# Optimization experiments

Measured on AMD Instinct MI355X. Metric: run time of the kernel, lower is better.

## Reference

```python
import jax, jax.numpy as jnp
import numpy as np

IN_C, OUT_C, N = 512, 256, 8192
NEG_INF = -1000000000.0  # matches torch's -1e9 fill


def setup_inputs() -> dict:
    key = jax.random.key(0)
    ks = jax.random.split(key, 8)
    x = jax.random.normal(ks[0], (N, IN_C), dtype=jnp.float32)
    adj = jax.random.randint(ks[1], (N, N), 0, 2, dtype=jnp.int32)
    # fc: Linear(in_c, out_c)
    lim_fc = 1.0 / np.sqrt(IN_C)
    W_fc = jax.random.uniform(ks[2], (IN_C, OUT_C), minval=-lim_fc, maxval=lim_fc, dtype=jnp.float32)
    b_fc = jax.random.uniform(ks[3], (OUT_C,), minval=-lim_fc, maxval=lim_fc, dtype=jnp.float32)
    # a1, a2: Linear(out_c, 1)
    lim_a = 1.0 / np.sqrt(OUT_C)
    W_a1 = jax.random.uniform(ks[4], (OUT_C, 1), minval=-lim_a, maxval=lim_a, dtype=jnp.float32)
    b_a1 = jax.random.uniform(ks[5], (1,), minval=-lim_a, maxval=lim_a, dtype=jnp.float32)
    W_a2 = jax.random.uniform(ks[6], (OUT_C, 1), minval=-lim_a, maxval=lim_a, dtype=jnp.float32)
    b_a2 = jax.random.uniform(ks[7], (1,), minval=-lim_a, maxval=lim_a, dtype=jnp.float32)
    return {"x": x, "adj": adj, "W_fc": W_fc, "b_fc": b_fc,
            "W_a1": W_a1, "b_a1": b_a1, "W_a2": W_a2, "b_a2": b_a2}


def reference(x, adj, W_fc, b_fc, W_a1, b_a1, W_a2, b_a2):
    h = x @ W_fc + b_fc                      # [N, out_c]
    s1 = h @ W_a1 + b_a1                     # [N, 1]
    s2 = h @ W_a2 + b_a2                     # [N, 1]
    e = jax.nn.leaky_relu(s1 + s2.T)         # [N, N], slope 0.01 matches torch default
    att = jnp.where(adj > 0, e, NEG_INF)
    att = jax.nn.softmax(att, axis=1)        # dropout omitted (eval mode)
    return att @ h                           # [N, out_c]
```

## Files before the change

kernel.cpp:

```cpp
#include <hip/hip_runtime.h>
#include <hip/hip_bf16.h>

#define IN_C 512
#define OUT_C 256
#define NN 8192
#define JSPL 4
#define JRANGE (NN / JSPL)
#define NT (JRANGE / 64)

typedef __attribute__((ext_vector_type(8))) short s16x8;
typedef __attribute__((ext_vector_type(4))) float f32x4;

__device__ __forceinline__ ushort f2bf(float f) {
    unsigned u = __float_as_uint(f);
    unsigned r = (u + 0x7FFF + ((u >> 16) & 1)) >> 16;
    return (ushort)r;
}

__device__ __forceinline__ void gload_lds16(const uint4* g, uint4* l) {
    __builtin_amdgcn_global_load_lds(
        (const __attribute__((address_space(1))) unsigned int*)g,
        (__attribute__((address_space(3))) unsigned int*)l, 16, 0, 0);
}

__global__ __launch_bounds__(256) void fc_kernel(
    const float* __restrict__ x, const float* __restrict__ Wfc,
    const float* __restrict__ bfc, const float* __restrict__ Wa1,
    const float* __restrict__ ba1, const float* __restrict__ Wa2,
    const float* __restrict__ ba2,
    uint4* __restrict__ hb,
    float* __restrict__ s1, float* __restrict__ s2)
{
    __shared__ float xl[8 * IN_C];
    __shared__ float red[2][8][4];
    const int t = threadIdx.x;
    const int r0 = blockIdx.x * 8;

    {
        const float4* src = (const float4*)(x + (size_t)r0 * IN_C);
        float4* dst = (float4*)xl;
        #pragma unroll
        for (int i = 0; i < 4; i++) dst[i * 256 + t] = src[i * 256 + t];
    }
    __syncthreads();

    float acc[8];
    #pragma unroll
    for (int r = 0; r < 8; r++) acc[r] = 0.f;

    for (int c4 = 0; c4 < IN_C / 4; c4++) {
        const float w0 = Wfc[(c4 * 4 + 0) * OUT_C + t];
        const float w1 = Wfc[(c4 * 4 + 1) * OUT_C + t];
        const float w2 = Wfc[(c4 * 4 + 2) * OUT_C + t];
        const float w3 = Wfc[(c4 * 4 + 3) * OUT_C + t];
        #pragma unroll
        for (int r = 0; r < 8; r++) {
            const float4 xv = *(const float4*)&xl[r * IN_C + c4 * 4];
            acc[r] = fmaf(xv.x, w0, acc[r]);
            acc[r] = fmaf(xv.y, w1, acc[r]);
            acc[r] = fmaf(xv.z, w2, acc[r]);
            acc[r] = fmaf(xv.w, w3, acc[r]);
        }
    }
    const float bb = bfc[t];
    #pragma unroll
    for (int r = 0; r < 8; r++) acc[r] += bb;

    {
        union { ushort u[8]; uint4 v; } pk;
        #pragma unroll
        for (int r = 0; r < 8; r++) pk.u[r] = f2bf(acc[r]);
        const int jt = r0 >> 6, u = (r0 >> 3) & 7;
        hb[(size_t)jt * 2048 + t * 8 + (u ^ (t & 7))] = pk.v;
    }

    float p1[8], p2[8];
    const float wa1 = Wa1[t], wa2 = Wa2[t];
    #pragma unroll
    for (int r = 0; r < 8; r++) { p1[r] = acc[r] * wa1; p2[r] = acc[r] * wa2; }
    #pragma unroll
    for (int off = 32; off > 0; off >>= 1) {
        #pragma unroll
        for (int r = 0; r < 8; r++) {
            p1[r] += __shfl_down(p1[r], off);
            p2[r] += __shfl_down(p2[r], off);
        }
    }
    const int wv = t >> 6, ln = t & 63;
    if (ln == 0) {
        #pragma unroll
        for (int r = 0; r < 8; r++) { red[0][r][wv] = p1[r]; red[1][r][wv] = p2[r]; }
    }
    __syncthreads();
    if (t < 16) {
        const int s = t >> 3, r = t & 7;
        float v = red[s][r][0] + red[s][r][1] + red[s][r][2] + red[s][r][3];
        v += s ? ba2[0] : ba1[0];
        if (s) s2[r0 + r] = v; else s1[r0 + r] = v;
    }
}

__global__ __launch_bounds__(256) void smax_kernel(const float* __restrict__ s2,
                                                   float* __restrict__ smax)
{
    __shared__ float red[4];
    float m = -1e30f;
    for (int i = threadIdx.x; i < NN; i += 256) m = fmaxf(m, s2[i]);
    #pragma unroll
    for (int off = 32; off > 0; off >>= 1) m = fmaxf(m, __shfl_down(m, off));
    if ((threadIdx.x & 63) == 0) red[threadIdx.x >> 6] = m;
    __syncthreads();
    if (threadIdx.x == 0)
        smax[0] = fmaxf(fmaxf(red[0], red[1]), fmaxf(red[2], red[3]));
}

__global__ __launch_bounds__(256, 2) void attn_kernel(
    const int* __restrict__ adj, const uint4* __restrict__ hb,
    const float* __restrict__ s1, const float* __restrict__ s2,
    const float* __restrict__ smaxp, float* __restrict__ outp,
    float* __restrict__ pbase, float* __restrict__ rs)
{
    __shared__ float s2l[JRANGE];
    __shared__ uint4 hbuf[2][2048];

    const int t = threadIdx.x;
    const int wave = t >> 6, lane = t & 63;
    const int g = lane >> 4, lr = lane & 15;
    const int jq = blockIdx.y;
    const int Jbase = jq * JRANGE;
    const int row = blockIdx.x * 64 + wave * 16 + lr;

    {
        const float4* src = (const float4*)(s2 + Jbase);
        float4* dst = (float4*)s2l;
        #pragma unroll
        for (int i = 0; i < JRANGE / 4 / 256; i++) dst[i * 256 + t] = src[i * 256 + t];
    }

    const float my_s1 = s1[row];
    const float z0 = my_s1 + smaxp[0];
    const float m_i = fmaxf(z0, 0.01f * z0);

    f32x4 acc[16];
    #pragma unroll
    for (int n = 0; n < 16; n++) acc[n] = (f32x4)(0.f);
    float rsum = 0.f;

    const int* adj_row = adj + (size_t)row * NN + Jbase + g * 8;
    const uint4* hb_base = hb + (size_t)(Jbase >> 6) * 2048;
    const int stidx = wave * 512 + lane;

    #pragma unroll
    for (int u = 0; u < 8; u++)
        gload_lds16(hb_base + stidx + u * 64, &hbuf[0][stidx + u * 64]);
    int4 ap0 = *(const int4*)(adj_row);
    int4 ap1 = *(const int4*)(adj_row + 4);
    int4 ap2 = *(const int4*)(adj_row + 32);
    int4 ap3 = *(const int4*)(adj_row + 36);
    __syncthreads();

    for (int tt = 0; tt < NT; ++tt) {
        const int cur = tt & 1;
        const bool more = (tt + 1 < NT);
        if (more) {
            const uint4* gs = hb_base + (size_t)(tt + 1) * 2048 + stidx;
            #pragma unroll
            for (int u = 0; u < 8; u++)
                gload_lds16(gs + u * 64, &hbuf[cur ^ 1][stidx + u * 64]);
        }
        const int av[16] = {ap0.x, ap0.y, ap0.z, ap0.w, ap1.x, ap1.y, ap1.z, ap1.w,
                            ap2.x, ap2.y, ap2.z, ap2.w, ap3.x, ap3.y, ap3.z, ap3.w};
        if (more) {
            const int* anx = adj_row + (tt + 1) * 64;
            ap0 = *(const int4*)(anx);
            ap1 = *(const int4*)(anx + 4);
            ap2 = *(const int4*)(anx + 32);
            ap3 = *(const int4*)(anx + 36);
        }

        const int J = tt * 64;
        #pragma unroll
        for (int s = 0; s < 2; s++) {
            const int j0 = J + s * 32 + g * 8;
            const float4 sva = *(const float4*)(s2l + j0);
            const float4 svb = *(const float4*)(s2l + j0 + 4);
            const float sv[8] = {sva.x, sva.y, sva.z, sva.w, svb.x, svb.y, svb.z, svb.w};
            union { ushort u[8]; s16x8 v; } pk;
            #pragma unroll
            for (int e = 0; e < 8; e++) {
                const float zz = my_s1 + sv[e];
                const float ee = fmaxf(zz, 0.01f * zz);
                float p = __expf(ee - m_i);
                p = (av[s * 8 + e] > 0) ? p : 0.f;
                rsum += p;
                pk.u[e] = f2bf(p);
            }
            const s16x8 afrag = pk.v;
            const int slot = (s * 4 + g) ^ (lr & 7);
            #pragma unroll
            for (int n = 0; n < 16; n++) {
                const int col = n * 16 + lr;
                const s16x8 bfrag = *(const s16x8*)&hbuf[cur][col * 8 + slot];
                acc[n] = __builtin_amdgcn_mfma_f32_16x16x32_bf16(afrag, bfrag, acc[n], 0, 0, 0);
            }
        }
        __syncthreads();
    }

    rsum += __shfl_xor(rsum, 16);
    rsum += __shfl_xor(rsum, 32);
    if (g == 0) rs[(size_t)jq * NN + row] = rsum;

    float* dst = (jq == 0) ? outp : (pbase + (size_t)(jq - 1) * ((size_t)NN * OUT_C));
    #pragma unroll
    for (int r = 0; r < 4; r++) {
        const int orow = blockIdx.x * 64 + wave * 16 + g * 4 + r;
        float* op = dst + (size_t)orow * OUT_C + lr;
        #pragma unroll
        for (int n = 0; n < 16; n++) op[n * 16] = acc[n][r];
    }
}

__global__ __launch_bounds__(256) void combine_kernel(
    float* __restrict__ out, const float* __restrict__ pbase,
    const float* __restrict__ rs)
{
    const int row = blockIdx.x, t = threadIdx.x;
    const float rsum = rs[row] + rs[NN + row] + rs[2 * NN + row] + rs[3 * NN + row];
    const float inv = 1.f / rsum;
    const size_t idx = (size_t)row * OUT_C + t;
    const size_t stride = (size_t)NN * OUT_C;
    const float v = out[idx] + pbase[idx] + pbase[idx + stride] + pbase[idx + 2 * stride];
    out[idx] = v * inv;
}

extern "C" void kernel_launch(void* const* d_in, const int* in_sizes, int n_in,
                              void* d_out, int out_size, void* d_ws, size_t ws_size,
                              hipStream_t stream) {
    const float* x   = (const float*)d_in[0];
    const int*   adj = (const int*)d_in[1];
    const float* Wfc = (const float*)d_in[2];
    const float* bfc = (const float*)d_in[3];
    const float* Wa1 = (const float*)d_in[4];
    const float* ba1 = (const float*)d_in[5];
    const float* Wa2 = (const float*)d_in[6];
    const float* ba2 = (const float*)d_in[7];
    float* out = (float*)d_out;

    char* ws = (char*)d_ws;
    uint4* hb   = (uint4*)ws;
    float* s1   = (float*)(ws + (4u << 20));
    float* s2   = s1 + NN;
    float* rs   = s2 + NN;
    float* smax = rs + 4 * NN;
    float* pbase = (float*)(ws + (5u << 20));

    fc_kernel<<<dim3(NN / 8), 256, 0, stream>>>(x, Wfc, bfc, Wa1, ba1, Wa2, ba2, hb, s1, s2);
    smax_kernel<<<dim3(1), 256, 0, stream>>>(s2, smax);
    attn_kernel<<<dim3(NN / 64, JSPL), 256, 0, stream>>>(adj, hb, s1, s2, smax, out, pbase, rs);
    combine_kernel<<<dim3(NN), 256, 0, stream>>>(out, pbase, rs);
}
```

Before: 180.0 us.

## Pack adjacency matrix into a bitmask before the attention kernel

Measured after the change: 186.2 us. +3.5%, slower.

```diff
diff --git a/kernel.cpp b/kernel.cpp
--- a/kernel.cpp
+++ b/kernel.cpp
@@ -7,6 +7,7 @@
 #define JSPL 4
 #define JRANGE (NN / JSPL)
 #define NT (JRANGE / 64)
+#define CHUNKS_TOTAL (NN * (NN / 256))
 
 typedef __attribute__((ext_vector_type(8))) short s16x8;
 typedef __attribute__((ext_vector_type(4))) float f32x4;
@@ -21,6 +22,26 @@
     __builtin_amdgcn_global_load_lds(
         (const __attribute__((address_space(1))) unsigned int*)g,
         (__attribute__((address_space(3))) unsigned int*)l, 16, 0, 0);
+}
+
+__global__ __launch_bounds__(256) void pack_kernel(const int* __restrict__ adj,
+                                                   unsigned char* __restrict__ mask)
+{
+    const int wid = blockIdx.x * 4 + (threadIdx.x >> 6);
+    const int lane = threadIdx.x & 63;
+    const size_t base = (size_t)wid * 64;
+    #pragma unroll 4
+    for (int i = 0; i < 64; i++) {
+        const size_t ci = base + i;
+        const int4 a = ((const int4*)adj)[ci * 64 + lane];
+        unsigned nib = (unsigned)(a.x > 0)
+                     | ((unsigned)(a.y > 0) << 1)
+                     | ((unsigned)(a.z > 0) << 2)
+                     | ((unsigned)(a.w > 0) << 3);
+        const unsigned other = (unsigned)__shfl_xor((int)nib, 1);
+        const unsigned byte = nib | (other << 4);
+        if (!(lane & 1)) mask[ci * 32 + (lane >> 1)] = (unsigned char)byte;
+    }
 }
 
 __global__ __launch_bounds__(256) void fc_kernel(
@@ -115,7 +136,7 @@
 }
 
 __global__ __launch_bounds__(256, 2) void attn_kernel(
-    const int* __restrict__ adj, const uint4* __restrict__ hb,
+    const unsigned long long* __restrict__ mask, const uint4* __restrict__ hb,
     const float* __restrict__ s1, const float* __restrict__ s2,
     const float* __restrict__ smaxp, float* __restrict__ outp,
     float* __restrict__ pbase, float* __restrict__ rs)
@@ -146,17 +167,14 @@
     for (int n = 0; n < 16; n++) acc[n] = (f32x4)(0.f);
     float rsum = 0.f;
 
-    const int* adj_row = adj + (size_t)row * NN + Jbase + g * 8;
+    const unsigned long long* mrow = mask + (size_t)row * (NN / 64) + (Jbase >> 6);
     const uint4* hb_base = hb + (size_t)(Jbase >> 6) * 2048;
     const int stidx = wave * 512 + lane;
 
     #pragma unroll
     for (int u = 0; u < 8; u++)
         gload_lds16(hb_base + stidx + u * 64, &hbuf[0][stidx + u * 64]);
-    int4 ap0 = *(const int4*)(adj_row);
-    int4 ap1 = *(const int4*)(adj_row + 4);
-    int4 ap2 = *(const int4*)(adj_row + 32);
-    int4 ap3 = *(const int4*)(adj_row + 36);
+    unsigned long long mp = mrow[0];
     __syncthreads();
 
     for (int tt = 0; tt < NT; ++tt) {
@@ -168,20 +186,14 @@
             for (int u = 0; u < 8; u++)
                 gload_lds16(gs + u * 64, &hbuf[cur ^ 1][stidx + u * 64]);
         }
-        const int av[16] = {ap0.x, ap0.y, ap0.z, ap0.w, ap1.x, ap1.y, ap1.z, ap1.w,
-                            ap2.x, ap2.y, ap2.z, ap2.w, ap3.x, ap3.y, ap3.z, ap3.w};
-        if (more) {
-            const int* anx = adj_row + (tt + 1) * 64;
-            ap0 = *(const int4*)(anx);
-            ap1 = *(const int4*)(anx + 4);
-            ap2 = *(const int4*)(anx + 32);
-            ap3 = *(const int4*)(anx + 36);
-        }
+        const unsigned long long m64 = mp;
+        if (more) mp = mrow[tt + 1];
 
         const int J = tt * 64;
         #pragma unroll
         for (int s = 0; s < 2; s++) {
             const int j0 = J + s * 32 + g * 8;
+            const unsigned mb = (unsigned)(m64 >> (s * 32 + g * 8)) & 0xFFu;
             const float4 sva = *(const float4*)(s2l + j0);
             const float4 svb = *(const float4*)(s2l + j0 + 4);
             const float sv[8] = {sva.x, sva.y, sva.z, sva.w, svb.x, svb.y, svb.z, svb.w};
@@ -191,7 +203,7 @@
                 const float zz = my_s1 + sv[e];
                 const float ee = fmaxf(zz, 0.01f * zz);
                 float p = __expf(ee - m_i);
-                p = (av[s * 8 + e] > 0) ? p : 0.f;
+                p = ((mb >> e) & 1u) ? p : 0.f;
                 rsum += p;
                 pk.u[e] = f2bf(p);
             }
@@ -254,9 +266,12 @@
     float* rs   = s2 + NN;
     float* smax = rs + 4 * NN;
     float* pbase = (float*)(ws + (5u << 20));
-
+    unsigned char* mask = (unsigned char*)(ws + (29u << 20));
+
+    pack_kernel<<<dim3(1024), 256, 0, stream>>>(adj, mask);
     fc_kernel<<<dim3(NN / 8), 256, 0, stream>>>(x, Wfc, bfc, Wa1, ba1, Wa2, ba2, hb, s1, s2);
     smax_kernel<<<dim3(1), 256, 0, stream>>>(s2, smax);
-    attn_kernel<<<dim3(NN / 64, JSPL), 256, 0, stream>>>(adj, hb, s1, s2, smax, out, pbase, rs);
+    attn_kernel<<<dim3(NN / 64, JSPL), 256, 0, stream>>>((const unsigned long long*)mask,
+                                                         hb, s1, s2, smax, out, pbase, rs);
     combine_kernel<<<dim3(NN), 256, 0, stream>>>(out, pbase, rs);
 }
```

## Prepass adjacency into LDS bitmasks and shrink h tiles to 32 columns

Applied to the files above, without the earlier changes.

Measured after the change: 189.4 us. 5.2% more time.

```diff
diff --git a/kernel.cpp b/kernel.cpp
--- a/kernel.cpp
+++ b/kernel.cpp
@@ -6,7 +6,7 @@
 #define NN 8192
 #define JSPL 4
 #define JRANGE (NN / JSPL)
-#define NT (JRANGE / 64)
+#define NT (JRANGE / 32)
 
 typedef __attribute__((ext_vector_type(8))) short s16x8;
 typedef __attribute__((ext_vector_type(4))) float f32x4;
@@ -70,8 +70,8 @@
         union { ushort u[8]; uint4 v; } pk;
         #pragma unroll
         for (int r = 0; r < 8; r++) pk.u[r] = f2bf(acc[r]);
-        const int jt = r0 >> 6, u = (r0 >> 3) & 7;
-        hb[(size_t)jt * 2048 + t * 8 + (u ^ (t & 7))] = pk.v;
+        const int jt = r0 >> 5, u = (r0 >> 3) & 3;
+        hb[(size_t)jt * 1024 + u * 256 + t] = pk.v;
     }
 
     float p1[8], p2[8];
@@ -121,14 +121,22 @@
     float* __restrict__ pbase, float* __restrict__ rs)
 {
     __shared__ float s2l[JRANGE];
-    __shared__ uint4 hbuf[2][2048];
+    __shared__ uint4 hbuf[2][1024];
+    __shared__ unsigned long long mask_lds[64][33];
 
     const int t = threadIdx.x;
     const int wave = t >> 6, lane = t & 63;
     const int g = lane >> 4, lr = lane & 15;
     const int jq = blockIdx.y;
     const int Jbase = jq * JRANGE;
-    const int row = blockIdx.x * 64 + wave * 16 + lr;
+    const int R0 = blockIdx.x * 64;
+    const int row = R0 + wave * 16 + lr;
+
+    const uint4* hb_base = hb + (size_t)(Jbase >> 5) * 1024;
+
+    #pragma unroll
+    for (int q = 0; q < 4; q++)
+        gload_lds16(hb_base + q * 256 + t, &hbuf[0][q * 256 + t]);
 
     {
         const float4* src = (const float4*)(s2 + Jbase);
@@ -136,6 +144,22 @@
         #pragma unroll
         for (int i = 0; i < JRANGE / 4 / 256; i++) dst[i * 256 + t] = src[i * 256 + t];
     }
+
+    {
+        const int* abase = adj + (size_t)(R0 + wave * 16) * NN + Jbase + lane;
+        for (int c = 0; c < 32; ++c) {
+            int v[16];
+            #pragma unroll
+            for (int r = 0; r < 16; ++r)
+                v[r] = __builtin_nontemporal_load(abase + (size_t)r * NN + c * 64);
+            #pragma unroll
+            for (int r = 0; r < 16; ++r) {
+                const unsigned long long m = __ballot(v[r] > 0);
+                if (lane == 0) mask_lds[wave * 16 + r][c] = m;
+            }
+        }
+    }
+    __syncthreads();
 
     const float my_s1 = s1[row];
     const float z0 = my_s1 + smaxp[0];
@@ -145,64 +169,39 @@
     #pragma unroll
     for (int n = 0; n < 16; n++) acc[n] = (f32x4)(0.f);
     float rsum = 0.f;
-
-    const int* adj_row = adj + (size_t)row * NN + Jbase + g * 8;
-    const uint4* hb_base = hb + (size_t)(Jbase >> 6) * 2048;
-    const int stidx = wave * 512 + lane;
-
-    #pragma unroll
-    for (int u = 0; u < 8; u++)
-        gload_lds16(hb_base + stidx + u * 64, &hbuf[0][stidx + u * 64]);
-    int4 ap0 = *(const int4*)(adj_row);
-    int4 ap1 = *(const int4*)(adj_row + 4);
-    int4 ap2 = *(const int4*)(adj_row + 32);
-    int4 ap3 = *(const int4*)(adj_row + 36);
-    __syncthreads();
 
     for (int tt = 0; tt < NT; ++tt) {
         const int cur = tt & 1;
         const bool more = (tt + 1 < NT);
         if (more) {
-            const uint4* gs = hb_base + (size_t)(tt + 1) * 2048 + stidx;
+            const uint4* gs = hb_base + (size_t)(tt + 1) * 1024;
             #pragma unroll
-            for (int u = 0; u < 8; u++)
-                gload_lds16(gs + u * 64, &hbuf[cur ^ 1][stidx + u * 64]);
-        }
-        const int av[16] = {ap0.x, ap0.y, ap0.z, ap0.w, ap1.x, ap1.y, ap1.z, ap1.w,
-                            ap2.x, ap2.y, ap2.z, ap2.w, ap3.x, ap3.y, ap3.z, ap3.w};
-        if (more) {
-            const int* anx = adj_row + (tt + 1) * 64;
-            ap0 = *(const int4*)(anx);
-            ap1 = *(const int4*)(anx + 4);
-            ap2 = *(const int4*)(anx + 32);
-            ap3 = *(const int4*)(anx + 36);
-        }
-
-        const int J = tt * 64;
-        #pragma unroll
-        for (int s = 0; s < 2; s++) {
-            const int j0 = J + s * 32 + g * 8;
-            const float4 sva = *(const float4*)(s2l + j0);
-            const float4 svb = *(const float4*)(s2l + j0 + 4);
-            const float sv[8] = {sva.x, sva.y, sva.z, sva.w, svb.x, svb.y, svb.z, svb.w};
-            union { ushort u[8]; s16x8 v; } pk;
-            #pragma unroll
-            for (int e = 0; e < 8; e++) {
-                const float zz = my_s1 + sv[e];
-                const float ee = fmaxf(zz, 0.01f * zz);
-                float p = __expf(ee - m_i);
-                p = (av[s * 8 + e] > 0) ? p : 0.f;
-                rsum += p;
-                pk.u[e] = f2bf(p);
-            }
-            const s16x8 afrag = pk.v;
-            const int slot = (s * 4 + g) ^ (lr & 7);
-            #pragma unroll
-            for (int n = 0; n < 16; n++) {
-                const int col = n * 16 + lr;
-                const s16x8 bfrag = *(const s16x8*)&hbuf[cur][col * 8 + slot];
-                acc[n] = __builtin_amdgcn_mfma_f32_16x16x32_bf16(afrag, bfrag, acc[n], 0, 0, 0);
-            }
+            for (int q = 0; q < 4; q++)
+                gload_lds16(gs + q * 256 + t, &hbuf[cur ^ 1][q * 256 + t]);
+        }
+
+        const unsigned long long m64 = mask_lds[wave * 16 + lr][tt >> 1];
+        const unsigned mb = (unsigned)(m64 >> ((tt & 1) * 32 + g * 8)) & 0xFFu;
+
+        const int j0 = tt * 32 + g * 8;
+        const float4 sva = *(const float4*)(s2l + j0);
+        const float4 svb = *(const float4*)(s2l + j0 + 4);
+        const float sv[8] = {sva.x, sva.y, sva.z, sva.w, svb.x, svb.y, svb.z, svb.w};
+        union { ushort u[8]; s16x8 v; } pk;
+        #pragma unroll
+        for (int e = 0; e < 8; e++) {
+            const float zz = my_s1 + sv[e];
+            const float ee = fmaxf(zz, 0.01f * zz);
+            float p = __expf(ee - m_i);
+            p = ((mb >> e) & 1u) ? p : 0.f;
+            rsum += p;
+            pk.u[e] = f2bf(p);
+        }
+        const s16x8 afrag = pk.v;
+        #pragma unroll
+        for (int n = 0; n < 16; n++) {
+            const s16x8 bfrag = *(const s16x8*)&hbuf[cur][g * 256 + n * 16 + lr];
+            acc[n] = __builtin_amdgcn_mfma_f32_16x16x32_bf16(afrag, bfrag, acc[n], 0, 0, 0);
         }
         __syncthreads();
     }
@@ -214,7 +213,7 @@
     float* dst = (jq == 0) ? outp : (pbase + (size_t)(jq - 1) * ((size_t)NN * OUT_C));
     #pragma unroll
     for (int r = 0; r < 4; r++) {
-        const int orow = blockIdx.x * 64 + wave * 16 + g * 4 + r;
+        const int orow = R0 + wave * 16 + g * 4 + r;
         float* op = dst + (size_t)orow * OUT_C + lr;
         #pragma unroll
         for (int n = 0; n < 16; n++) op[n * 16] = acc[n][r];
```
